# Kernel optimization log

Hardware: AMD Instinct MI355X
Metric: run time of the kernel (lower is better)

Reference implementation:

```python
import jax, jax.numpy as jnp
import numpy as np

B, CIN, REL, OUT, SH, H, W = 8, 256, 16, 64, 8, 56, 56
HW = H * W
K = 7          # window size
DIL = 2        # dilation
EPS = 1e-5


def conv1x1(x, w, b=None):
    # x: [B,C,h,w], w: [O,C]
    y = jnp.einsum('oc,bchw->bohw', w, x)
    if b is not None:
        y = y + b[None, :, None, None]
    return y


def bn_eval(x, g, b, m, v):
    scale = g / jnp.sqrt(v + EPS)
    return x * scale[None, :, None, None] + (b - m * scale)[None, :, None, None]


def unfold49(x, pad_reflect, pad_zero):
    # x: [B,C,H,W] -> [B,C,49,H,W]; 7x7 window, dilation 2, stride 1.
    if pad_reflect:
        x = jnp.pad(x, ((0, 0), (0, 0), (pad_reflect, pad_reflect), (pad_reflect, pad_reflect)), mode='reflect')
    if pad_zero:
        x = jnp.pad(x, ((0, 0), (0, 0), (pad_zero, pad_zero), (pad_zero, pad_zero)))
    patches = [x[:, :, DIL * i:DIL * i + H, DIL * j:DIL * j + W]
               for i in range(K) for j in range(K)]
    return jnp.stack(patches, axis=2)


def setup_inputs() -> dict:
    key = jax.random.key(0)
    ks = jax.random.split(key, 12)
    s_in = 1.0 / np.sqrt(CIN)
    inp = {
        'x': jax.random.normal(ks[0], (B, CIN, H, W), jnp.float32),
        'w1': jax.random.normal(ks[1], (REL, CIN), jnp.float32) * s_in,
        'b1': jax.random.normal(ks[2], (REL,), jnp.float32) * 0.01,
        'w2': jax.random.normal(ks[3], (REL, CIN), jnp.float32) * s_in,
        'b2': jax.random.normal(ks[4], (REL,), jnp.float32) * 0.01,
        'w3': jax.random.normal(ks[5], (OUT, CIN), jnp.float32) * s_in,
        'b3': jax.random.normal(ks[6], (OUT,), jnp.float32) * 0.01,
        'bn1_g': jax.random.uniform(ks[7], (REL * (K * K + 1),), jnp.float32, 0.5, 1.5),
        'bn1_b': jax.random.normal(ks[8], (REL * (K * K + 1),), jnp.float32) * 0.01,
        'bn1_m': jnp.zeros((REL * (K * K + 1),), jnp.float32),
        'bn1_v': jnp.ones((REL * (K * K + 1),), jnp.float32),
        'wcw1': jax.random.normal(ks[9], (OUT // SH, REL * (K * K + 1)), jnp.float32) * (1.0 / np.sqrt(REL * 50)),
        'bn2_g': jax.random.uniform(ks[10], (OUT // SH,), jnp.float32, 0.5, 1.5),
        'bn2_b': jnp.zeros((OUT // SH,), jnp.float32),
        'bn2_m': jnp.zeros((OUT // SH,), jnp.float32),
        'bn2_v': jnp.ones((OUT // SH,), jnp.float32),
        'wcw2': jax.random.normal(ks[11], (K * K * OUT // SH, OUT // SH), jnp.float32) * (1.0 / np.sqrt(OUT // SH)),
        'bcw2': jnp.zeros((K * K * OUT // SH,), jnp.float32),
    }
    return inp


def reference(x, w1, b1, w2, b2, w3, b3, bn1_g, bn1_b, bn1_m, bn1_v,
              wcw1, bn2_g, bn2_b, bn2_m, bn2_v, wcw2, bcw2):
    x1 = conv1x1(x, w1, b1)                      # [B,REL,H,W]
    x2 = conv1x1(x, w2, b2)                      # [B,REL,H,W]
    x3 = conv1x1(x, w3, b3)                      # [B,OUT,H,W]

    # x1 -> [B,REL,1,HW]
    x1f = x1.reshape(B, REL, 1, HW)
    # x2: ReflectionPad2d(2) then Unfold(7, dilation=2, padding=4) -> [B,REL*49,1,HW]
    x2u = unfold49(x2, pad_reflect=2, pad_zero=4).reshape(B, REL * K * K, 1, HW)

    cat = jnp.concatenate([x1f, x2u], axis=1)    # [B, REL*50, 1, HW]
    t = jax.nn.relu(bn_eval(cat, bn1_g, bn1_b, bn1_m, bn1_v))
    t = conv1x1(t, wcw1)                         # [B, OUT/SH, 1, HW], no bias
    t = jax.nn.relu(bn_eval(t, bn2_g, bn2_b, bn2_m, bn2_v))
    wmap = conv1x1(t, wcw2, bcw2)                # [B, 49*OUT/SH, 1, HW]
    wmap = wmap.reshape(B, OUT // SH, K * K, HW)  # channel layout wc*49+k

    # Aggregation(7, 1, 6, 2, pad_mode=1): reflect-pad 6, 7x7 dilated unfold,
    # out[b,c,n] = sum_k unf[b,c,k,n] * w[b, c//SH, k, n]
    x3u = unfold49(x3, pad_reflect=6, pad_zero=0).reshape(B, OUT // SH, SH, K * K, HW)
    out = jnp.einsum('bgskn,bgkn->bgsn', x3u, wmap).reshape(B, OUT, H, W)
    return out
```

## Files before the change

kernel.cpp:

```cpp
#include <hip/hip_runtime.h>
#include <hip/hip_bf16.h>

#define HW    3136
#define HH    56
#define NCIN  256
#define KK    49
#define PH    68
#define PP    (PH*PH)

#define OFF_WT    0
#define OFF_BCAT  24576
#define OFF_TAB   24672
#define OFF_WTAB  34272
#define OFF_B2F   38976
#define OFF_X1    39040
#define OFF_X2P   440448
#define OFF_X3P   1032320
#define OFF_TB    3399808

__global__ __launch_bounds__(256) void kprep(
    const float* __restrict__ w1, const float* __restrict__ b1,
    const float* __restrict__ w2, const float* __restrict__ b2,
    const float* __restrict__ w3, const float* __restrict__ b3,
    const float* __restrict__ bn1g, const float* __restrict__ bn1b,
    const float* __restrict__ bn1m, const float* __restrict__ bn1v,
    const float* __restrict__ wcw1,
    const float* __restrict__ bn2g, const float* __restrict__ bn2b,
    const float* __restrict__ bn2m, const float* __restrict__ bn2v,
    const float* __restrict__ wcw2, const float* __restrict__ bcw2,
    float* __restrict__ ws)
{
    int idx = blockIdx.x * 256 + threadIdx.x;
    if (idx < 24576) {
        int o = idx >> 8, c = idx & 255;
        float v = (o < 16) ? w1[o * 256 + c]
                : (o < 32) ? w2[(o - 16) * 256 + c]
                           : w3[(o - 32) * 256 + c];
        ws[OFF_WT + c * 96 + o] = v;
    }
    int i2 = idx - 24576;
    if (i2 >= 0 && i2 < 96) {
        float v = (i2 < 16) ? b1[i2] : (i2 < 32) ? b2[i2 - 16] : b3[i2 - 32];
        ws[OFF_BCAT + i2] = v;
    }
    int i3 = idx - 24672;
    if (i3 >= 0 && i3 < 9600) {
        int row = i3 / 12, c = i3 - row * 12;
        int uu = row >> 4, r = row & 15;
        int j = (uu < 49) ? (16 + r * KK + uu) : r;
        float val = 0.f;
        if (c == 0) {
            val = bn1g[j] / sqrtf(bn1v[j] + 1e-5f);
        } else if (c == 1) {
            float s = bn1g[j] / sqrtf(bn1v[j] + 1e-5f);
            val = bn1b[j] - bn1m[j] * s;
        } else if (c < 10) {
            int e = c - 2;
            float s2 = bn2g[e] / sqrtf(bn2v[e] + 1e-5f);
            val = wcw1[e * 800 + j] * s2;
        }
        ws[OFF_TAB + i3] = val;
    }
    int i4 = idx - 34272;
    if (i4 >= 0 && i4 < 4704) {
        int row = i4 / 12, c = i4 - row * 12;
        float val = 0.f;
        if (c == 0)      val = bcw2[row];
        else if (c < 9)  val = wcw2[row * 8 + (c - 1)];
        ws[OFF_WTAB + i4] = val;
    }
    int i5 = idx - 38976;
    if (i5 >= 0 && i5 < 8) {
        float s2 = bn2g[i5] / sqrtf(bn2v[i5] + 1e-5f);
        ws[OFF_B2F + i5] = bn2b[i5] - bn2m[i5] * s2;
    }
}

__global__ __launch_bounds__(512) void kconv(
    const float* __restrict__ x, const float* __restrict__ wT,
    const float* __restrict__ bcat, float* __restrict__ x1out,
    float* __restrict__ x2pad, float* __restrict__ x3pad)
{
    __shared__ float xl[64][64];
    const int tid = threadIdx.x;
    const int l   = tid & 63;
    const int wv  = __builtin_amdgcn_readfirstlane(tid >> 6);
    const int b   = blockIdx.x / 49;
    const int hw0 = (blockIdx.x % 49) * 64;
    const int ob  = wv * 12;

    {
        int z = (blockIdx.x % 49) * 336 + tid;
        if (tid < 336 && z < 16384) {
            int ch = z >> 10, cell = z & 1023;
            int p, q;
            if (cell < 272)      { p = cell / 68;          q = cell - p * 68; }
            else if (cell < 544) { int cc = cell - 272; p = 64 + cc / 68; q = cc - (p - 64) * 68; }
            else                 { int cc = cell - 544; p = 4 + (cc >> 3); int qq = cc & 7; q = (qq < 4) ? qq : 60 + qq; }
            x2pad[((size_t)b * 16 + ch) * PP + p * PH + q] = 0.f;
        }
    }

    float acc[12];
    const float* bc = bcat + ob;
#pragma unroll
    for (int i = 0; i < 12; ++i) acc[i] = bc[i];

    const float* xb = x + (size_t)b * NCIN * HW + hw0;

    for (int cc = 0; cc < 4; ++cc) {
        __syncthreads();
#pragma unroll
        for (int i = 0; i < 8; ++i)
            xl[i * 8 + wv][l] = xb[(size_t)(cc * 64 + i * 8 + wv) * HW + l];
        __syncthreads();

        const float* wp = wT + (cc * 64) * 96 + ob;
#pragma unroll 4
        for (int k = 0; k < 64; ++k) {
            float xv = xl[k][l];
            const float4* wq = (const float4*)(wp + k * 96);
            float4 A = wq[0], B = wq[1], C = wq[2];
            acc[0]  = fmaf(xv, A.x, acc[0]);  acc[1]  = fmaf(xv, A.y, acc[1]);
            acc[2]  = fmaf(xv, A.z, acc[2]);  acc[3]  = fmaf(xv, A.w, acc[3]);
            acc[4]  = fmaf(xv, B.x, acc[4]);  acc[5]  = fmaf(xv, B.y, acc[5]);
            acc[6]  = fmaf(xv, B.z, acc[6]);  acc[7]  = fmaf(xv, B.w, acc[7]);
            acc[8]  = fmaf(xv, C.x, acc[8]);  acc[9]  = fmaf(xv, C.y, acc[9]);
            acc[10] = fmaf(xv, C.z, acc[10]); acc[11] = fmaf(xv, C.w, acc[11]);
        }
    }

    const int n  = hw0 + l;
    const int y  = n / HH;
    const int xx = n - y * HH;
    const int p0 = y + 6, q0 = xx + 6;
    const int yr3 = (y >= 1 && y <= 6) ? 6 - y : ((y >= 49 && y <= 54) ? 116 - y : -1);
    const int xr3 = (xx >= 1 && xx <= 6) ? 6 - xx : ((xx >= 49 && xx <= 54) ? 116 - xx : -1);
    const int yr2 = (y == 1 || y == 2) ? 6 - y : ((y == 53 || y == 54) ? 116 - y : -1);
    const int xr2 = (xx == 1 || xx == 2) ? 6 - xx : ((xx == 53 || xx == 54) ? 116 - xx : -1);

#pragma unroll
    for (int i = 0; i < 12; ++i) {
        const int ch = ob + i;
        const float v = acc[i];
        if (ch < 16) {
            x1out[((size_t)b * 16 + ch) * HW + n] = v;
        } else if (ch < 32) {
            float* pl = x2pad + ((size_t)b * 16 + (ch - 16)) * PP;
            pl[p0 * PH + q0] = v;
            if (yr2 >= 0)              pl[yr2 * PH + q0]  = v;
            if (xr2 >= 0)              pl[p0 * PH + xr2]  = v;
            if (yr2 >= 0 && xr2 >= 0)  pl[yr2 * PH + xr2] = v;
        } else {
            float* pl = x3pad + ((size_t)b * 64 + (ch - 32)) * PP;
            pl[p0 * PH + q0] = v;
            if (yr3 >= 0)              pl[yr3 * PH + q0]  = v;
            if (xr3 >= 0)              pl[p0 * PH + xr3]  = v;
            if (yr3 >= 0 && xr3 >= 0)  pl[yr3 * PH + xr3] = v;
        }
    }
}

__global__ __launch_bounds__(1024, 8) void kt(
    const float* __restrict__ x1, const float* __restrict__ x2pad,
    const float* __restrict__ tab, const float* __restrict__ b2f,
    float* __restrict__ tbuf)
{
    __shared__ float red[16][8][64];
    const int tid = threadIdx.x;
    const int w   = __builtin_amdgcn_readfirstlane(tid >> 6);
    const int l   = tid & 63;
    const int b   = blockIdx.x / 49;
    const int nb  = (blockIdx.x % 49) * 64;
    const int n   = nb + l;
    const int y   = n / HH;
    const int xx  = n - y * HH;
    const int pbase = y * PH + xx;

    const float* x1b = x1 + (size_t)b * 16 * HW + n;
    const float* x2b = x2pad + (size_t)b * 16 * PP + pbase;

    float acc[8];
#pragma unroll
    for (int g = 0; g < 8; ++g) acc[g] = 0.f;

    const int u0 = (50 * w) >> 4;
    const int u1 = (50 * (w + 1)) >> 4;

#pragma unroll 1
    for (int u = u0; u < u1; ++u) {
        const float* trow;
        const float* xp;
        size_t xstr;
        if (u == 0) {
            trow = tab + 49 * 192;
            xp   = x1b;
            xstr = HW;
        } else {
            const int kk = u - 1;
            const int i  = kk / 7;
            const int jj = kk - i * 7;
            trow = tab + kk * 192;
            xp   = x2b + i * (2 * PH) + jj * 2;
            xstr = PP;
        }
#pragma unroll
        for (int r = 0; r < 16; ++r) {
            const float4* tq = (const float4*)(trow + r * 12);
            float4 A = tq[0], Bv = tq[1], Cv = tq[2];
            float v = xp[(size_t)r * xstr];
            v = fmaxf(fmaf(v, A.x, A.y), 0.f);
            acc[0] = fmaf(v, A.z, acc[0]);  acc[1] = fmaf(v, A.w, acc[1]);
            acc[2] = fmaf(v, Bv.x, acc[2]); acc[3] = fmaf(v, Bv.y, acc[3]);
            acc[4] = fmaf(v, Bv.z, acc[4]); acc[5] = fmaf(v, Bv.w, acc[5]);
            acc[6] = fmaf(v, Cv.x, acc[6]); acc[7] = fmaf(v, Cv.y, acc[7]);
        }
    }

#pragma unroll
    for (int g = 0; g < 8; ++g) red[w][g][l] = acc[g];
    __syncthreads();

    if (tid < 512) {
        const int g  = tid >> 6;
        const int px = tid & 63;
        float s = b2f[g];
#pragma unroll
        for (int sl = 0; sl < 16; ++sl) s += red[sl][g][px];
        tbuf[((size_t)b * 8 + g) * HW + nb + px] = fmaxf(s, 0.f);
    }
}

__global__ __launch_bounds__(1024, 8) void kagg(
    const float* __restrict__ x3pad, const float* __restrict__ tbuf,
    const float* __restrict__ wtab, float* __restrict__ out)
{
    __shared__ float red[8][8][64];
    const int tid  = threadIdx.x;
    const int wave = tid >> 6;
    const int g    = __builtin_amdgcn_readfirstlane(wave & 7);
    const int kh   = __builtin_amdgcn_readfirstlane(wave >> 3);
    const int l    = tid & 63;
    const int b    = blockIdx.x / 49;
    const int nb   = (blockIdx.x % 49) * 64;
    const int n    = nb + l;
    const int y    = n / HH;
    const int xx   = n - y * HH;
    const int pbase = y * PH + xx;

    float t[8];
#pragma unroll
    for (int e = 0; e < 8; ++e) t[e] = tbuf[((size_t)b * 8 + e) * HW + n];

    float acc[8];
#pragma unroll
    for (int s = 0; s < 8; ++s) acc[s] = 0.f;

    const float* x3b = x3pad + ((size_t)b * 64 + g * 8) * PP + pbase;
    const float* wg  = wtab + (size_t)g * KK * 12;

    const int k0 = kh * 25;
    const int k1 = kh ? KK : 25;

#pragma unroll 1
    for (int k = k0; k < k1; ++k) {
        const int i  = k / 7;
        const int jj = k - i * 7;
        const float* wrow = wg + k * 12;
        const float4* wq = (const float4*)wrow;
        float4 A = wq[0], Bv = wq[1];
        float w7 = wrow[8];
        float wv = A.x;
        wv = fmaf(t[0], A.y, wv);  wv = fmaf(t[1], A.z, wv);
        wv = fmaf(t[2], A.w, wv);  wv = fmaf(t[3], Bv.x, wv);
        wv = fmaf(t[4], Bv.y, wv); wv = fmaf(t[5], Bv.z, wv);
        wv = fmaf(t[6], Bv.w, wv); wv = fmaf(t[7], w7, wv);

        const float* xp = x3b + i * (2 * PH) + jj * 2;
#pragma unroll
        for (int s = 0; s < 8; ++s)
            acc[s] = fmaf(xp[(size_t)s * PP], wv, acc[s]);
    }

    if (kh == 1) {
#pragma unroll
        for (int s = 0; s < 8; ++s) red[g][s][l] = acc[s];
    }
    __syncthreads();
    if (kh == 0) {
        float* op = out + ((size_t)b * 64 + g * 8) * HW + n;
#pragma unroll
        for (int s = 0; s < 8; ++s)
            op[(size_t)s * HW] = acc[s] + red[g][s][l];
    }
}

extern "C" void kernel_launch(void* const* d_in, const int* in_sizes, int n_in,
                              void* d_out, int out_size, void* d_ws, size_t ws_size,
                              hipStream_t stream) {
    const float* x    = (const float*)d_in[0];
    const float* w1   = (const float*)d_in[1];
    const float* b1   = (const float*)d_in[2];
    const float* w2   = (const float*)d_in[3];
    const float* b2   = (const float*)d_in[4];
    const float* w3   = (const float*)d_in[5];
    const float* b3   = (const float*)d_in[6];
    const float* bn1g = (const float*)d_in[7];
    const float* bn1b = (const float*)d_in[8];
    const float* bn1m = (const float*)d_in[9];
    const float* bn1v = (const float*)d_in[10];
    const float* wcw1 = (const float*)d_in[11];
    const float* bn2g = (const float*)d_in[12];
    const float* bn2b = (const float*)d_in[13];
    const float* bn2m = (const float*)d_in[14];
    const float* bn2v = (const float*)d_in[15];
    const float* wcw2 = (const float*)d_in[16];
    const float* bcw2 = (const float*)d_in[17];

    float* ws = (float*)d_ws;

    kprep<<<153, 256, 0, stream>>>(w1, b1, w2, b2, w3, b3,
                                   bn1g, bn1b, bn1m, bn1v, wcw1,
                                   bn2g, bn2b, bn2m, bn2v, wcw2, bcw2, ws);
    kconv<<<392, 512, 0, stream>>>(x, ws + OFF_WT, ws + OFF_BCAT,
                                   ws + OFF_X1, ws + OFF_X2P, ws + OFF_X3P);
    kt<<<392, 1024, 0, stream>>>(ws + OFF_X1, ws + OFF_X2P,
                                 ws + OFF_TAB, ws + OFF_B2F, ws + OFF_TB);
    kagg<<<392, 1024, 0, stream>>>(ws + OFF_X3P, ws + OFF_TB,
                                   ws + OFF_WTAB, (float*)d_out);
}
```

Before: 81.42 us.

## Fuse weight-map and aggregation kernels into one block with LDS handoff

Merges the kernel that computes the per-pixel 8-channel hidden map with the aggregation kernel into one 512-thread kernel. The hidden map is kept in shared memory instead of a global buffer, which removes a launch and a global round trip. The aggregation is remapped so each lane handles two adjacent pixels and four output channels with float2 loads and stores, covering all 49 taps per wave with no cross-wave reduction. In exchange each block has half the threads, the first stage has twice the serial work per wave, and register pressure is higher.

```diff
diff --git a/kernel.cpp b/kernel.cpp
--- a/kernel.cpp
+++ b/kernel.cpp
@@ -16,7 +16,6 @@
 #define OFF_X1    39040
 #define OFF_X2P   440448
 #define OFF_X3P   1032320
-#define OFF_TB    3399808
 
 __global__ __launch_bounds__(256) void kprep(
     const float* __restrict__ w1, const float* __restrict__ b1,
@@ -161,12 +160,14 @@
     }
 }
 
-__global__ __launch_bounds__(1024, 8) void kt(
+__global__ __launch_bounds__(512) void kmainB(
     const float* __restrict__ x1, const float* __restrict__ x2pad,
-    const float* __restrict__ tab, const float* __restrict__ b2f,
-    float* __restrict__ tbuf)
+    const float* __restrict__ x3pad, const float* __restrict__ tab,
+    const float* __restrict__ b2f, const float* __restrict__ wtab,
+    float* __restrict__ out)
 {
-    __shared__ float red[16][8][64];
+    __shared__ float red[8][8][64];
+    __shared__ float tl[8][64];
     const int tid = threadIdx.x;
     const int w   = __builtin_amdgcn_readfirstlane(tid >> 6);
     const int l   = tid & 63;
@@ -184,8 +185,8 @@
 #pragma unroll
     for (int g = 0; g < 8; ++g) acc[g] = 0.f;
 
-    const int u0 = (50 * w) >> 4;
-    const int u1 = (50 * (w + 1)) >> 4;
+    const int u0 = (50 * w) >> 3;
+    const int u1 = (50 * (w + 1)) >> 3;
 
 #pragma unroll 1
     for (int u = u0; u < u1; ++u) {
@@ -221,78 +222,70 @@
     for (int g = 0; g < 8; ++g) red[w][g][l] = acc[g];
     __syncthreads();
 
-    if (tid < 512) {
+    {
         const int g  = tid >> 6;
         const int px = tid & 63;
         float s = b2f[g];
 #pragma unroll
-        for (int sl = 0; sl < 16; ++sl) s += red[sl][g][px];
-        tbuf[((size_t)b * 8 + g) * HW + nb + px] = fmaxf(s, 0.f);
-    }
-}
-
-__global__ __launch_bounds__(1024, 8) void kagg(
-    const float* __restrict__ x3pad, const float* __restrict__ tbuf,
-    const float* __restrict__ wtab, float* __restrict__ out)
-{
-    __shared__ float red[8][8][64];
-    const int tid  = threadIdx.x;
-    const int wave = tid >> 6;
-    const int g    = __builtin_amdgcn_readfirstlane(wave & 7);
-    const int kh   = __builtin_amdgcn_readfirstlane(wave >> 3);
-    const int l    = tid & 63;
-    const int b    = blockIdx.x / 49;
-    const int nb   = (blockIdx.x % 49) * 64;
-    const int n    = nb + l;
-    const int y    = n / HH;
-    const int xx   = n - y * HH;
-    const int pbase = y * PH + xx;
-
-    float t[8];
-#pragma unroll
-    for (int e = 0; e < 8; ++e) t[e] = tbuf[((size_t)b * 8 + e) * HW + n];
-
-    float acc[8];
-#pragma unroll
-    for (int s = 0; s < 8; ++s) acc[s] = 0.f;
-
-    const float* x3b = x3pad + ((size_t)b * 64 + g * 8) * PP + pbase;
+        for (int ww = 0; ww < 8; ++ww) s += red[ww][g][px];
+        tl[g][px] = fmaxf(s, 0.f);
+    }
+    __syncthreads();
+
+    const int g   = w;
+    const int sh  = l >> 5;
+    const int pp2 = l & 31;
+    const int n0  = nb + pp2 * 2;
+    const int y0  = n0 / HH;
+    const int xx0 = n0 - y0 * HH;
+    const int pb2 = y0 * PH + xx0;
+
+    float t0[8], t1[8];
+#pragma unroll
+    for (int e = 0; e < 8; ++e) {
+        t0[e] = tl[e][pp2 * 2];
+        t1[e] = tl[e][pp2 * 2 + 1];
+    }
+
+    float2 acc2[4];
+#pragma unroll
+    for (int s = 0; s < 4; ++s) acc2[s] = make_float2(0.f, 0.f);
+
+    const float* x3b = x3pad + ((size_t)b * 64 + g * 8 + sh * 4) * PP + pb2;
     const float* wg  = wtab + (size_t)g * KK * 12;
 
-    const int k0 = kh * 25;
-    const int k1 = kh ? KK : 25;
-
 #pragma unroll 1
-    for (int k = k0; k < k1; ++k) {
-        const int i  = k / 7;
-        const int jj = k - i * 7;
-        const float* wrow = wg + k * 12;
-        const float4* wq = (const float4*)wrow;
-        float4 A = wq[0], Bv = wq[1];
-        float w7 = wrow[8];
-        float wv = A.x;
-        wv = fmaf(t[0], A.y, wv);  wv = fmaf(t[1], A.z, wv);
-        wv = fmaf(t[2], A.w, wv);  wv = fmaf(t[3], Bv.x, wv);
-        wv = fmaf(t[4], Bv.y, wv); wv = fmaf(t[5], Bv.z, wv);
-        wv = fmaf(t[6], Bv.w, wv); wv = fmaf(t[7], w7, wv);
-
-        const float* xp = x3b + i * (2 * PH) + jj * 2;
-#pragma unroll
-        for (int s = 0; s < 8; ++s)
-            acc[s] = fmaf(xp[(size_t)s * PP], wv, acc[s]);
-    }
-
-    if (kh == 1) {
-#pragma unroll
-        for (int s = 0; s < 8; ++s) red[g][s][l] = acc[s];
-    }
-    __syncthreads();
-    if (kh == 0) {
-        float* op = out + ((size_t)b * 64 + g * 8) * HW + n;
-#pragma unroll
-        for (int s = 0; s < 8; ++s)
-            op[(size_t)s * HW] = acc[s] + red[g][s][l];
-    }
+    for (int i = 0; i < 7; ++i) {
+        const float* xrow = x3b + i * (2 * PH);
+#pragma unroll
+        for (int jj = 0; jj < 7; ++jj) {
+            const int k = i * 7 + jj;
+            const float* wrow = wg + k * 12;
+            const float4* wq = (const float4*)wrow;
+            float4 A = wq[0], Bv = wq[1];
+            float w7 = wrow[8];
+            float w0 = A.x, w1 = A.x;
+            w0 = fmaf(t0[0], A.y, w0);  w1 = fmaf(t1[0], A.y, w1);
+            w0 = fmaf(t0[1], A.z, w0);  w1 = fmaf(t1[1], A.z, w1);
+            w0 = fmaf(t0[2], A.w, w0);  w1 = fmaf(t1[2], A.w, w1);
+            w0 = fmaf(t0[3], Bv.x, w0); w1 = fmaf(t1[3], Bv.x, w1);
+            w0 = fmaf(t0[4], Bv.y, w0); w1 = fmaf(t1[4], Bv.y, w1);
+            w0 = fmaf(t0[5], Bv.z, w0); w1 = fmaf(t1[5], Bv.z, w1);
+            w0 = fmaf(t0[6], Bv.w, w0); w1 = fmaf(t1[6], Bv.w, w1);
+            w0 = fmaf(t0[7], w7, w0);   w1 = fmaf(t1[7], w7, w1);
+#pragma unroll
+            for (int s = 0; s < 4; ++s) {
+                float2 xv = *(const float2*)(xrow + (size_t)s * PP + jj * 2);
+                acc2[s].x = fmaf(xv.x, w0, acc2[s].x);
+                acc2[s].y = fmaf(xv.y, w1, acc2[s].y);
+            }
+        }
+    }
+
+    float* op = out + ((size_t)b * 64 + g * 8 + sh * 4) * HW + n0;
+#pragma unroll
+    for (int s = 0; s < 4; ++s)
+        *(float2*)(op + (size_t)s * HW) = acc2[s];
 }
 
 extern "C" void kernel_launch(void* const* d_in, const int* in_sizes, int n_in,
@@ -324,8 +317,7 @@
                                    bn2g, bn2b, bn2m, bn2v, wcw2, bcw2, ws);
     kconv<<<392, 512, 0, stream>>>(x, ws + OFF_WT, ws + OFF_BCAT,
                                    ws + OFF_X1, ws + OFF_X2P, ws + OFF_X3P);
-    kt<<<392, 1024, 0, stream>>>(ws + OFF_X1, ws + OFF_X2P,
-                                 ws + OFF_TAB, ws + OFF_B2F, ws + OFF_TB);
-    kagg<<<392, 1024, 0, stream>>>(ws + OFF_X3P, ws + OFF_TB,
-                                   ws + OFF_WTAB, (float*)d_out);
+    kmainB<<<392, 512, 0, stream>>>(ws + OFF_X1, ws + OFF_X2P, ws + OFF_X3P,
+                                    ws + OFF_TAB, ws + OFF_B2F, ws + OFF_WTAB,
+                                    (float*)d_out);
 }
```

After: 71.29 us, median of 2. 1.14x faster.
